# Kernel optimization log

Hardware: AMD Instinct MI355X
Metric: run time of the kernel (lower is better)

The kernel has to match this reference:

```python
import jax, jax.numpy as jnp
import numpy as np

N_NODES = 10000
N_EDGES = 320000
D_IN = 256
D_OUT = 256
NEG_SLOPE = 0.2


def setup_inputs() -> dict:
    key = jax.random.key(0)
    ks = jax.random.split(key, 8)
    feature = jax.random.normal(ks[0], (N_NODES, D_IN), dtype=jnp.float32)
    src = jax.random.randint(ks[1], (N_EDGES,), 0, N_NODES, dtype=jnp.int32)
    dst = jax.random.randint(ks[2], (N_EDGES,), 0, N_NODES, dtype=jnp.int32)
    # Xavier-ish scaled weights
    s = 1.0 / np.sqrt(D_IN)
    W_s = jax.random.normal(ks[3], (D_OUT, D_IN), dtype=jnp.float32) * s
    W_t = jax.random.normal(ks[4], (D_OUT, D_IN), dtype=jnp.float32) * s
    W_attn = jax.random.normal(ks[5], (1, D_OUT), dtype=jnp.float32) * (1.0 / np.sqrt(D_OUT))
    W_fc = jax.random.normal(ks[6], (D_OUT, D_IN), dtype=jnp.float32) * s
    b_fc = jnp.zeros((D_OUT,), dtype=jnp.float32)
    return {"feature": feature, "src": src, "dst": dst,
            "W_s": W_s, "W_t": W_t, "W_attn": W_attn,
            "W_fc": W_fc, "b_fc": b_fc}


def reference(feature, src, dst, W_s, W_t, W_attn, W_fc, b_fc):
    n = feature.shape[0]
    # Project at node level, then gather (same math as projecting gathered feats).
    proj_s = feature @ W_s.T          # [N, D_OUT]
    proj_t = feature @ W_t.T          # [N, D_OUT]
    # Edge attention logits: attn(LeakyReLU(h_dst + h_src))
    z = proj_s[src] + proj_t[dst]     # [E, D_OUT]
    z = jnp.where(z >= 0, z, NEG_SLOPE * z)
    e = (z @ W_attn.T)[:, 0]          # [E]
    # edge_softmax with norm_by='src': softmax over outgoing edges of each src node
    m = jax.ops.segment_max(e, src, num_segments=n)          # [N]
    m = jnp.where(jnp.isfinite(m), m, 0.0)                   # guard empty segments
    e_exp = jnp.exp(e - m[src])                               # [E]
    denom = jax.ops.segment_sum(e_exp, src, num_segments=n)  # [N]
    alpha = e_exp / denom[src]                                # [E]
    # message = src feature * alpha; reduce = sum at dst
    msg = feature[src] * alpha[:, None]                       # [E, D_IN]
    agg = jax.ops.segment_sum(msg, dst, num_segments=n)       # [N, D_IN]
    # final linear
    return agg @ W_fc.T + b_fc
```

## Files before the change

kernel.cpp:

```cpp
#include <hip/hip_runtime.h>
#include <math.h>

#define N_NODES 10000
#define N_EDGES 320000
#define D 256
#define NEG_SLOPE 0.2f
#define BCAP 96
#define BLOCK 256
#define NF4 (N_NODES * D / 4)
#define NW4 (256 * 256 / 4)
#define NTILE_M 157
#define NTILES (NTILE_M * 12)
#define FILL_BLOCKS ((N_EDGES + BLOCK - 1) / BLOCK)
#define APAD 264

typedef unsigned short ushortT;
typedef __attribute__((ext_vector_type(8))) short bf16x8;
typedef __attribute__((ext_vector_type(4))) float f32x4;

__device__ __forceinline__ unsigned short f2bf(float f) {
  unsigned int u = __float_as_uint(f);
  u += 0x7FFFu + ((u >> 16) & 1u);
  return (unsigned short)(u >> 16);
}
__device__ __forceinline__ float bf2f(unsigned short u) {
  return __uint_as_float((unsigned int)u << 16);
}

__global__ void prep_kernel(const float* __restrict__ feat,
                            const float* __restrict__ Ws,
                            const float* __restrict__ Wt,
                            const float* __restrict__ Wfc,
                            ushortT* __restrict__ featb,
                            ushortT* __restrict__ Wcat,
                            int* __restrict__ cnt,
                            float* __restrict__ denom) {
  const int g = blockIdx.x * blockDim.x + threadIdx.x;
  if (g < NF4) {
    float4 v = ((const float4*)feat)[g];
    ushort4 u;
    u.x = f2bf(v.x); u.y = f2bf(v.y); u.z = f2bf(v.z); u.w = f2bf(v.w);
    ((ushort4*)featb)[g] = u;
    return;
  }
  const int gi = g - NF4;
  if (gi < 3 * NW4) {
    const float* W = (gi < NW4) ? Ws : ((gi < 2 * NW4) ? Wt : Wfc);
    const int off = gi - ((gi < NW4) ? 0 : ((gi < 2 * NW4) ? NW4 : 2 * NW4));
    float4 v = ((const float4*)W)[off];
    ushort4 u;
    u.x = f2bf(v.x); u.y = f2bf(v.y); u.z = f2bf(v.z); u.w = f2bf(v.w);
    ((ushort4*)Wcat)[gi] = u;
    return;
  }
  const int gn = gi - 3 * NW4;
  if (gn < N_NODES) {
    cnt[gn] = 0;
    denom[gn] = 0.f;
  }
}

__global__ __launch_bounds__(256, 4) void proj_fill_kernel(
    const ushortT* __restrict__ featb,
    const ushortT* __restrict__ Wcat,
    const int* __restrict__ src, const int* __restrict__ dst,
    int* __restrict__ cnt, int* __restrict__ src_b,
    ushortT* __restrict__ ps, ushortT* __restrict__ pt,
    ushortT* __restrict__ fcp) {
  __shared__ ushortT Als[64][APAD];

  if (blockIdx.x < FILL_BLOCKS) {
    const int i = blockIdx.x * BLOCK + threadIdx.x;
    if (i < N_EDGES) {
      const int dn = dst[i];
      const int slot = atomicAdd(&cnt[dn], 1);
      if (slot < BCAP) src_b[dn * BCAP + slot] = src[i];
    }
    return;
  }
  const int p = blockIdx.x - FILL_BLOCKS;
  const int m0 = (p / 12) * 64;
  const int by = p % 12;
  ushortT* outp = (by < 4) ? ps : ((by < 8) ? pt : fcp);
  const int col0 = (by & 3) * 64;
  const int n0 = by * 64;

  const int tid = threadIdx.x;
  const int wave = tid >> 6;
  const int lane = tid & 63;
  const int quad = lane >> 4;
  const int l16 = lane & 15;

  const int m_base_t = (wave & 1) * 32;
  const int wn = wave >> 1;
  const int nb = n0 + wn * 32;

  bf16x8 b0r[8], b1r[8];
#pragma unroll
  for (int kk = 0; kk < 8; ++kk) {
    const int ko = kk * 32 + quad * 8;
    b0r[kk] = *(const bf16x8*)(Wcat + (size_t)(nb + l16) * D + ko);
    b1r[kk] = *(const bf16x8*)(Wcat + (size_t)(nb + 16 + l16) * D + ko);
  }

  const int tr = tid >> 2;
  const int tk = (tid & 3) * 64;
  const int gr = m0 + tr;
  const bf16x8 zero8 = {0, 0, 0, 0, 0, 0, 0, 0};
#pragma unroll
  for (int i = 0; i < 8; ++i) {
    bf16x8 av = (gr < N_NODES) ? *(const bf16x8*)(featb + (size_t)gr * D + tk + 8 * i) : zero8;
    *(bf16x8*)&Als[tr][tk + 8 * i] = av;
  }
  __builtin_amdgcn_sched_barrier(0);
  __syncthreads();

  f32x4 acc[2][2];
#pragma unroll
  for (int i = 0; i < 2; ++i)
#pragma unroll
    for (int j = 0; j < 2; ++j) acc[i][j] = (f32x4){0.f, 0.f, 0.f, 0.f};

  const int ar0 = m_base_t + l16;
#pragma unroll
  for (int kk = 0; kk < 8; ++kk) {
    const int ko = kk * 32 + quad * 8;
    bf16x8 a0 = *(const bf16x8*)&Als[ar0][ko];
    bf16x8 a1 = *(const bf16x8*)&Als[ar0 + 16][ko];
    acc[0][0] = __builtin_amdgcn_mfma_f32_16x16x32_bf16(a0, b0r[kk], acc[0][0], 0, 0, 0);
    acc[0][1] = __builtin_amdgcn_mfma_f32_16x16x32_bf16(a0, b1r[kk], acc[0][1], 0, 0, 0);
    acc[1][0] = __builtin_amdgcn_mfma_f32_16x16x32_bf16(a1, b0r[kk], acc[1][0], 0, 0, 0);
    acc[1][1] = __builtin_amdgcn_mfma_f32_16x16x32_bf16(a1, b1r[kk], acc[1][1], 0, 0, 0);
  }

#pragma unroll
  for (int mi = 0; mi < 2; ++mi) {
#pragma unroll
    for (int r = 0; r < 4; ++r) {
      const int row = m0 + m_base_t + mi * 16 + quad * 4 + r;
      if (row < N_NODES) {
#pragma unroll
        for (int ni = 0; ni < 2; ++ni) {
          const int col = col0 + wn * 32 + ni * 16 + l16;
          outp[(size_t)row * D + col] = f2bf(acc[mi][ni][r]);
        }
      }
    }
  }
}

__global__ __launch_bounds__(256) void logit_bucket_kernel(
    const ushortT* __restrict__ ps,
    const ushortT* __restrict__ pt,
    const int* __restrict__ cnt,
    const int* __restrict__ src_b,
    const float* __restrict__ Wattn,
    float* __restrict__ expv_b,
    float* __restrict__ denom) {
  const int n = blockIdx.x;
  const int cn = min(cnt[n], BCAP);
  if (cn == 0) return;
  const int wave = threadIdx.x >> 6;
  const int lane = threadIdx.x & 63;
  const int half = lane >> 5;
  const int l32 = lane & 31;
  const int grp = wave * 2 + half;
  const int base = n * BCAP;

  bf16x8 bu = *(const bf16x8*)(pt + (size_t)n * D + l32 * 8);
  float b[8], w[8];
  const float4 w0 = *(const float4*)(Wattn + l32 * 8);
  const float4 w1 = *(const float4*)(Wattn + l32 * 8 + 4);
  w[0] = w0.x; w[1] = w0.y; w[2] = w0.z; w[3] = w0.w;
  w[4] = w1.x; w[5] = w1.y; w[6] = w1.z; w[7] = w1.w;
#pragma unroll
  for (int i = 0; i < 8; ++i) b[i] = bf2f((unsigned short)bu[i]);

  int j = grp;
  for (; j + 24 < cn; j += 32) {
    const int s0 = src_b[base + j];
    const int s1 = src_b[base + j + 8];
    const int s2 = src_b[base + j + 16];
    const int s3 = src_b[base + j + 24];
    bf16x8 au0 = *(const bf16x8*)(ps + (size_t)s0 * D + l32 * 8);
    bf16x8 au1 = *(const bf16x8*)(ps + (size_t)s1 * D + l32 * 8);
    bf16x8 au2 = *(const bf16x8*)(ps + (size_t)s2 * D + l32 * 8);
    bf16x8 au3 = *(const bf16x8*)(ps + (size_t)s3 * D + l32 * 8);
    float sum0 = 0.f, sum1 = 0.f, sum2 = 0.f, sum3 = 0.f;
#pragma unroll
    for (int i = 0; i < 8; ++i) {
      float z0 = bf2f((unsigned short)au0[i]) + b[i];
      float z1 = bf2f((unsigned short)au1[i]) + b[i];
      float z2 = bf2f((unsigned short)au2[i]) + b[i];
      float z3 = bf2f((unsigned short)au3[i]) + b[i];
      z0 = fmaxf(z0, NEG_SLOPE * z0);
      z1 = fmaxf(z1, NEG_SLOPE * z1);
      z2 = fmaxf(z2, NEG_SLOPE * z2);
      z3 = fmaxf(z3, NEG_SLOPE * z3);
      sum0 = fmaf(w[i], z0, sum0);
      sum1 = fmaf(w[i], z1, sum1);
      sum2 = fmaf(w[i], z2, sum2);
      sum3 = fmaf(w[i], z3, sum3);
    }
#pragma unroll
    for (int off = 16; off > 0; off >>= 1) {
      sum0 += __shfl_down(sum0, off, 32);
      sum1 += __shfl_down(sum1, off, 32);
      sum2 += __shfl_down(sum2, off, 32);
      sum3 += __shfl_down(sum3, off, 32);
    }
    if (l32 == 0) {
      float ex0 = __expf(sum0), ex1 = __expf(sum1);
      float ex2 = __expf(sum2), ex3 = __expf(sum3);
      expv_b[base + j] = ex0;
      expv_b[base + j + 8] = ex1;
      expv_b[base + j + 16] = ex2;
      expv_b[base + j + 24] = ex3;
      atomicAdd(&denom[s0], ex0);
      atomicAdd(&denom[s1], ex1);
      atomicAdd(&denom[s2], ex2);
      atomicAdd(&denom[s3], ex3);
    }
  }
  for (; j < cn; j += 8) {
    const int s = src_b[base + j];
    bf16x8 au = *(const bf16x8*)(ps + (size_t)s * D + l32 * 8);
    float sum = 0.f;
#pragma unroll
    for (int i = 0; i < 8; ++i) {
      float z = bf2f((unsigned short)au[i]) + b[i];
      z = fmaxf(z, NEG_SLOPE * z);
      sum = fmaf(w[i], z, sum);
    }
#pragma unroll
    for (int off = 16; off > 0; off >>= 1) sum += __shfl_down(sum, off, 32);
    if (l32 == 0) {
      float ex = __expf(sum);
      expv_b[base + j] = ex;
      atomicAdd(&denom[s], ex);
    }
  }
}

__global__ __launch_bounds__(64) void prescale_kernel(
    const ushortT* __restrict__ fcp,
    const float* __restrict__ denom,
    ushortT* __restrict__ fcpsb) {
  const int n = blockIdx.x;
  const int t = threadIdx.x;
  const float inv = 1.0f / denom[n];
  ushort4 v = ((const ushort4*)(fcp + (size_t)n * D))[t];
  ushort4 o;
  o.x = f2bf(bf2f(v.x) * inv);
  o.y = f2bf(bf2f(v.y) * inv);
  o.z = f2bf(bf2f(v.z) * inv);
  o.w = f2bf(bf2f(v.w) * inv);
  ((ushort4*)(fcpsb + (size_t)n * D))[t] = o;
}

__global__ __launch_bounds__(256) void gather_agg_kernel(
    const ushortT* __restrict__ fcpsb,
    const int* __restrict__ cnt,
    const int* __restrict__ src_b,
    const float* __restrict__ expv_b,
    const float* __restrict__ b_fc,
    float* __restrict__ out) {
  __shared__ float red[8][D];
  const int n = blockIdx.x;
  const int tid = threadIdx.x;
  const int wave = tid >> 6;
  const int lane = tid & 63;
  const int half = lane >> 5;
  const int l32 = lane & 31;
  const int grp = wave * 2 + half;
  const int cn = min(cnt[n], BCAP);
  const int base = n * BCAP;

  float acc[8];
#pragma unroll
  for (int i = 0; i < 8; ++i) acc[i] = 0.f;

  int j = grp;
  for (; j + 24 < cn; j += 32) {
    const int s0 = src_b[base + j];
    const int s1 = src_b[base + j + 8];
    const int s2 = src_b[base + j + 16];
    const int s3 = src_b[base + j + 24];
    const float a0 = expv_b[base + j];
    const float a1 = expv_b[base + j + 8];
    const float a2 = expv_b[base + j + 16];
    const float a3 = expv_b[base + j + 24];
    bf16x8 f0 = *(const bf16x8*)(fcpsb + (size_t)s0 * D + l32 * 8);
    bf16x8 f1 = *(const bf16x8*)(fcpsb + (size_t)s1 * D + l32 * 8);
    bf16x8 f2 = *(const bf16x8*)(fcpsb + (size_t)s2 * D + l32 * 8);
    bf16x8 f3 = *(const bf16x8*)(fcpsb + (size_t)s3 * D + l32 * 8);
#pragma unroll
    for (int i = 0; i < 8; ++i) {
      acc[i] = fmaf(a0, bf2f((unsigned short)f0[i]), acc[i]);
      acc[i] = fmaf(a1, bf2f((unsigned short)f1[i]), acc[i]);
      acc[i] = fmaf(a2, bf2f((unsigned short)f2[i]), acc[i]);
      acc[i] = fmaf(a3, bf2f((unsigned short)f3[i]), acc[i]);
    }
  }
  for (; j < cn; j += 8) {
    const int s = src_b[base + j];
    const float a = expv_b[base + j];
    bf16x8 fu = *(const bf16x8*)(fcpsb + (size_t)s * D + l32 * 8);
#pragma unroll
    for (int i = 0; i < 8; ++i)
      acc[i] = fmaf(a, bf2f((unsigned short)fu[i]), acc[i]);
  }
  *(float4*)&red[grp][l32 * 8] = make_float4(acc[0], acc[1], acc[2], acc[3]);
  *(float4*)&red[grp][l32 * 8 + 4] = make_float4(acc[4], acc[5], acc[6], acc[7]);
  __syncthreads();
  float o = b_fc[tid];
#pragma unroll
  for (int g = 0; g < 8; ++g) o += red[g][tid];
  out[(size_t)n * D + tid] = o;
}

extern "C" void kernel_launch(void* const* d_in, const int* in_sizes, int n_in,
                              void* d_out, int out_size, void* d_ws, size_t ws_size,
                              hipStream_t stream) {
  const float* feat  = (const float*)d_in[0];
  const int*   src   = (const int*)d_in[1];
  const int*   dst   = (const int*)d_in[2];
  const float* Ws    = (const float*)d_in[3];
  const float* Wt    = (const float*)d_in[4];
  const float* Wattn = (const float*)d_in[5];
  const float* Wfc   = (const float*)d_in[6];
  const float* bfc   = (const float*)d_in[7];
  float* out = (float*)d_out;

  ushortT* ps    = (ushortT*)d_ws;
  ushortT* pt    = ps + (size_t)N_NODES * D;
  ushortT* fcp   = pt + (size_t)N_NODES * D;
  ushortT* featb = fcp + (size_t)N_NODES * D;
  ushortT* Wcat  = featb + (size_t)N_NODES * D;
  float* expv_b  = (float*)(Wcat + (size_t)768 * 256);
  float* denom   = expv_b + (size_t)N_NODES * BCAP;
  int*   cnt     = (int*)(denom + N_NODES);
  int*   src_b   = cnt + N_NODES;
  ushortT* fcpsb = featb;

  const int prep_items = NF4 + 3 * NW4 + N_NODES;
  prep_kernel<<<(prep_items + BLOCK - 1) / BLOCK, BLOCK, 0, stream>>>(
      feat, Ws, Wt, Wfc, featb, Wcat, cnt, denom);
  proj_fill_kernel<<<FILL_BLOCKS + NTILES, BLOCK, 0, stream>>>(
      featb, Wcat, src, dst, cnt, src_b, ps, pt, fcp);
  logit_bucket_kernel<<<N_NODES, BLOCK, 0, stream>>>(ps, pt, cnt, src_b, Wattn, expv_b, denom);
  prescale_kernel<<<N_NODES, 64, 0, stream>>>(fcp, denom, fcpsb);
  gather_agg_kernel<<<N_NODES, BLOCK, 0, stream>>>(fcpsb, cnt, src_b, expv_b, bfc, out);
}
```

Measured before the change: 178.6 us.

## Split edge fill from projection GEMM and stage weight tile in shared memory

The fused fill+projection kernel is split into two launches: a plain edge-bucketing kernel and a projection GEMM kernel. The GEMM now cooperatively loads the 64x256 weight tile into LDS alongside the feature tile, instead of each wave holding 16 weight vectors in registers from strided global loads. Launch bounds drop to 2 blocks per CU because LDS usage doubles. This cuts register pressure and redundant global weight loads, but adds a kernel launch and removes the overlap between the atomic fill and the GEMM.

```diff
diff --git a/kernel.cpp b/kernel.cpp
--- a/kernel.cpp
+++ b/kernel.cpp
@@ -60,25 +60,26 @@
   }
 }
 
-__global__ __launch_bounds__(256, 4) void proj_fill_kernel(
+__global__ void fill_kernel(const int* __restrict__ src,
+                            const int* __restrict__ dst,
+                            int* __restrict__ cnt,
+                            int* __restrict__ src_b) {
+  const int i = blockIdx.x * blockDim.x + threadIdx.x;
+  if (i >= N_EDGES) return;
+  const int dn = dst[i];
+  const int slot = atomicAdd(&cnt[dn], 1);
+  if (slot < BCAP) src_b[dn * BCAP + slot] = src[i];
+}
+
+__global__ __launch_bounds__(256, 2) void proj_kernel(
     const ushortT* __restrict__ featb,
     const ushortT* __restrict__ Wcat,
-    const int* __restrict__ src, const int* __restrict__ dst,
-    int* __restrict__ cnt, int* __restrict__ src_b,
     ushortT* __restrict__ ps, ushortT* __restrict__ pt,
     ushortT* __restrict__ fcp) {
   __shared__ ushortT Als[64][APAD];
-
-  if (blockIdx.x < FILL_BLOCKS) {
-    const int i = blockIdx.x * BLOCK + threadIdx.x;
-    if (i < N_EDGES) {
-      const int dn = dst[i];
-      const int slot = atomicAdd(&cnt[dn], 1);
-      if (slot < BCAP) src_b[dn * BCAP + slot] = src[i];
-    }
-    return;
-  }
-  const int p = blockIdx.x - FILL_BLOCKS;
+  __shared__ ushortT Bls[64][APAD];
+
+  const int p = blockIdx.x;
   const int m0 = (p / 12) * 64;
   const int by = p % 12;
   ushortT* outp = (by < 4) ? ps : ((by < 8) ? pt : fcp);
@@ -93,26 +94,23 @@
 
   const int m_base_t = (wave & 1) * 32;
   const int wn = wave >> 1;
-  const int nb = n0 + wn * 32;
-
-  bf16x8 b0r[8], b1r[8];
-#pragma unroll
-  for (int kk = 0; kk < 8; ++kk) {
-    const int ko = kk * 32 + quad * 8;
-    b0r[kk] = *(const bf16x8*)(Wcat + (size_t)(nb + l16) * D + ko);
-    b1r[kk] = *(const bf16x8*)(Wcat + (size_t)(nb + 16 + l16) * D + ko);
-  }
 
   const int tr = tid >> 2;
   const int tk = (tid & 3) * 64;
   const int gr = m0 + tr;
+  const int wr = n0 + tr;
   const bf16x8 zero8 = {0, 0, 0, 0, 0, 0, 0, 0};
-#pragma unroll
-  for (int i = 0; i < 8; ++i) {
-    bf16x8 av = (gr < N_NODES) ? *(const bf16x8*)(featb + (size_t)gr * D + tk + 8 * i) : zero8;
-    *(bf16x8*)&Als[tr][tk + 8 * i] = av;
-  }
-  __builtin_amdgcn_sched_barrier(0);
+  bf16x8 av[8], bv[8];
+#pragma unroll
+  for (int i = 0; i < 8; ++i)
+    av[i] = (gr < N_NODES) ? *(const bf16x8*)(featb + (size_t)gr * D + tk + 8 * i) : zero8;
+#pragma unroll
+  for (int i = 0; i < 8; ++i)
+    bv[i] = *(const bf16x8*)(Wcat + (size_t)wr * D + tk + 8 * i);
+#pragma unroll
+  for (int i = 0; i < 8; ++i) *(bf16x8*)&Als[tr][tk + 8 * i] = av[i];
+#pragma unroll
+  for (int i = 0; i < 8; ++i) *(bf16x8*)&Bls[tr][tk + 8 * i] = bv[i];
   __syncthreads();
 
   f32x4 acc[2][2];
@@ -122,15 +120,18 @@
     for (int j = 0; j < 2; ++j) acc[i][j] = (f32x4){0.f, 0.f, 0.f, 0.f};
 
   const int ar0 = m_base_t + l16;
+  const int br0 = wn * 32 + l16;
 #pragma unroll
   for (int kk = 0; kk < 8; ++kk) {
     const int ko = kk * 32 + quad * 8;
     bf16x8 a0 = *(const bf16x8*)&Als[ar0][ko];
     bf16x8 a1 = *(const bf16x8*)&Als[ar0 + 16][ko];
-    acc[0][0] = __builtin_amdgcn_mfma_f32_16x16x32_bf16(a0, b0r[kk], acc[0][0], 0, 0, 0);
-    acc[0][1] = __builtin_amdgcn_mfma_f32_16x16x32_bf16(a0, b1r[kk], acc[0][1], 0, 0, 0);
-    acc[1][0] = __builtin_amdgcn_mfma_f32_16x16x32_bf16(a1, b0r[kk], acc[1][0], 0, 0, 0);
-    acc[1][1] = __builtin_amdgcn_mfma_f32_16x16x32_bf16(a1, b1r[kk], acc[1][1], 0, 0, 0);
+    bf16x8 b0 = *(const bf16x8*)&Bls[br0][ko];
+    bf16x8 b1 = *(const bf16x8*)&Bls[br0 + 16][ko];
+    acc[0][0] = __builtin_amdgcn_mfma_f32_16x16x32_bf16(a0, b0, acc[0][0], 0, 0, 0);
+    acc[0][1] = __builtin_amdgcn_mfma_f32_16x16x32_bf16(a0, b1, acc[0][1], 0, 0, 0);
+    acc[1][0] = __builtin_amdgcn_mfma_f32_16x16x32_bf16(a1, b0, acc[1][0], 0, 0, 0);
+    acc[1][1] = __builtin_amdgcn_mfma_f32_16x16x32_bf16(a1, b1, acc[1][1], 0, 0, 0);
   }
 
 #pragma unroll
@@ -346,8 +347,8 @@
   const int prep_items = NF4 + 3 * NW4 + N_NODES;
   prep_kernel<<<(prep_items + BLOCK - 1) / BLOCK, BLOCK, 0, stream>>>(
       feat, Ws, Wt, Wfc, featb, Wcat, cnt, denom);
-  proj_fill_kernel<<<FILL_BLOCKS + NTILES, BLOCK, 0, stream>>>(
-      featb, Wcat, src, dst, cnt, src_b, ps, pt, fcp);
+  fill_kernel<<<FILL_BLOCKS, BLOCK, 0, stream>>>(src, dst, cnt, src_b);
+  proj_kernel<<<NTILES, BLOCK, 0, stream>>>(featb, Wcat, ps, pt, fcp);
   logit_bucket_kernel<<<N_NODES, BLOCK, 0, stream>>>(ps, pt, cnt, src_b, Wattn, expv_b, denom);
   prescale_kernel<<<N_NODES, 64, 0, stream>>>(fcp, denom, fcpsb);
   gather_agg_kernel<<<N_NODES, BLOCK, 0, stream>>>(fcpsb, cnt, src_b, expv_b, bfc, out);
```

Result: no change. 181.9 us (+1.8%).
